# Optimization experiments

Measured on AMD Instinct MI355X. Metric: run time of the kernel, lower is better.

Reference implementation:

```python
import jax, jax.numpy as jnp
import numpy as np

N_NODES = 50000
N_EDGES = 800000
IN_DIM = 128
HID = 128
OUT_DIM = 1
N_LAYERS = 3
NUM_GRAPHS = 500
LN_EPS = 1e-5


def setup_inputs() -> dict:
    key = jax.random.key(0)
    ks = jax.random.split(key, 16)
    x = jax.random.normal(ks[0], (N_NODES, IN_DIM), dtype=jnp.float32)
    edge_index = jax.random.randint(ks[1], (2, N_EDGES), 0, N_NODES, dtype=jnp.int32)
    batch = jnp.sort(jax.random.randint(ks[2], (N_NODES,), 0, NUM_GRAPHS, dtype=jnp.int32))
    s_in = 1.0 / np.sqrt(IN_DIM)
    s_h = 1.0 / np.sqrt(HID)
    W_in = jax.random.normal(ks[3], (HID, IN_DIM), jnp.float32) * s_in
    b_in = jnp.zeros((HID,), jnp.float32)
    Wc = jax.random.normal(ks[4], (N_LAYERS, HID, HID), jnp.float32) * s_h
    bc = jnp.zeros((N_LAYERS, HID), jnp.float32)
    gamma = jnp.ones((N_LAYERS, HID), jnp.float32)
    beta = jnp.zeros((N_LAYERS, HID), jnp.float32)
    W1 = jax.random.normal(ks[5], (HID // 2, HID), jnp.float32) * s_h
    b1 = jnp.zeros((HID // 2,), jnp.float32)
    W2 = jax.random.normal(ks[6], (OUT_DIM, HID // 2), jnp.float32) * (1.0 / np.sqrt(HID // 2))
    b2 = jnp.zeros((OUT_DIM,), jnp.float32)
    return dict(x=x, edge_index=edge_index, batch=batch, W_in=W_in, b_in=b_in,
                Wc=Wc, bc=bc, gamma=gamma, beta=beta, W1=W1, b1=b1, W2=W2, b2=b2)


def _layernorm(h, g, b):
    mu = jnp.mean(h, axis=-1, keepdims=True)
    var = jnp.mean(jnp.square(h - mu), axis=-1, keepdims=True)
    return (h - mu) * jax.lax.rsqrt(var + LN_EPS) * g + b


def reference(x, edge_index, batch, W_in, b_in, Wc, bc, gamma, beta, W1, b1, W2, b2):
    n = x.shape[0]
    src, dst = edge_index[0], edge_index[1]
    # GCN symmetric normalization with self-loops: deg_i = 1 + in-degree
    deg = jax.ops.segment_sum(jnp.ones_like(src, dtype=x.dtype), dst, num_segments=n) + 1.0
    dinv = jax.lax.rsqrt(deg)                       # [N]
    enorm = (dinv[src] * dinv[dst])[:, None]        # [E,1]
    self_norm = (dinv * dinv)[:, None]              # [N,1]

    h = x @ W_in.T + b_in                           # input projection [N,H]
    for l in range(N_LAYERS):
        res = h
        hw = h @ Wc[l].T                            # GCNConv linear (no bias)
        agg = jax.ops.segment_sum(hw[src] * enorm, dst, num_segments=n)
        agg = agg + hw * self_norm + bc[l]          # self-loop term + conv bias
        h = jax.nn.relu(_layernorm(agg, gamma[l], beta[l])) + res  # dropout is identity in eval

    # global_mean_pool
    counts = jax.ops.segment_sum(jnp.ones((n,), x.dtype), batch, num_segments=NUM_GRAPHS)
    pooled = jax.ops.segment_sum(h, batch, num_segments=NUM_GRAPHS) / jnp.maximum(counts, 1.0)[:, None]

    out = jax.nn.relu(pooled @ W1.T + b1) @ W2.T + b2
    return out
```

## Files before the change

### kernel.cpp

```cpp
#include <hip/hip_runtime.h>
#include <hip/hip_bf16.h>

#define HIDDIM 128
#define CAP 4096

typedef short bf16x8 __attribute__((ext_vector_type(8)));
typedef float f32x4 __attribute__((ext_vector_type(4)));

__device__ inline unsigned short f2bf(float f) {
    unsigned u = __float_as_uint(f);
    unsigned r = (u + 0x7fffu + ((u >> 16) & 1u)) >> 16;
    return (unsigned short)r;
}
__device__ inline float bf2f(unsigned short s) {
    return __uint_as_float(((unsigned)s) << 16);
}

__global__ __launch_bounds__(256) void preproc_misc(int* __restrict__ gcursor, int nbuck,
                                                    const int* __restrict__ batch, int n, int G,
                                                    int* __restrict__ gp,
                                                    const float* __restrict__ Win,
                                                    const float* __restrict__ Wc,
                                                    unsigned short* __restrict__ Wfrag,
                                                    int nbgp) {
    int bx = blockIdx.x;
    if (bx < 2) {
        int b = bx * 256 + threadIdx.x;
        if (b < nbuck) gcursor[b] = b * CAP;
        return;
    }
    bx -= 2;
    if (bx < nbgp) {
        int i = bx * 256 + threadIdx.x;
        if (i >= n) return;
        int bi = batch[i];
        if (i == 0) {
            for (int g = 0; g <= bi; ++g) gp[g] = 0;
        } else {
            int bp = batch[i - 1];
            for (int g = bp + 1; g <= bi; ++g) gp[g] = i;
        }
        if (i == n - 1) {
            for (int g = bi + 1; g <= G; ++g) gp[g] = n;
        }
        return;
    }
    bx -= nbgp;
    int gid = bx * 256 + threadIdx.x;
    if (gid >= 4 * 16384) return;
    int m = gid >> 14;
    int r = gid & 16383;
    int t = r >> 11;
    int kk = (r >> 9) & 3;
    int lane = (r >> 3) & 63;
    int j = r & 7;
    int kg = lane >> 4, oc = lane & 15;
    int o = t * 16 + oc;
    int k = kk * 32 + kg * 8 + j;
    const float* src = (m == 0) ? Win : (Wc + (m - 1) * 16384);
    float w = src[o * 128 + k];
    unsigned short hi = f2bf(w);
    unsigned short lo = f2bf(w - bf2f(hi));
    Wfrag[m * 32768 + r] = hi;
    Wfrag[m * 32768 + 16384 + r] = lo;
}

__global__ __launch_bounds__(256) void bucket_scatter(const int* __restrict__ ei, int E,
                                                      int* __restrict__ gcursor,
                                                      unsigned* __restrict__ ebuf, int nbuck) {
    __shared__ int lcount[512];
    __shared__ int lbase[512];
    int t = threadIdx.x;
    int cb = blockIdx.x * 2048;
    lcount[t] = 0;
    lcount[t + 256] = 0;
    __syncthreads();

    int bkt[8];
    int lpos[8];
    unsigned pk[8];
#pragma unroll
    for (int j = 0; j < 8; ++j) {
        int e = cb + j * 256 + t;
        if (e < E) {
            int s_ = ei[e];
            int d_ = ei[E + e];
            bkt[j] = d_ >> 7;
            pk[j] = ((unsigned)s_ << 7) | (unsigned)(d_ & 127);
            lpos[j] = atomicAdd(&lcount[bkt[j]], 1);
        } else {
            bkt[j] = -1;
            lpos[j] = 0;
            pk[j] = 0;
        }
    }
    __syncthreads();
    for (int bb = t; bb < nbuck; bb += 256) {
        int c = lcount[bb];
        lbase[bb] = c ? atomicAdd(&gcursor[bb], c) : 0;
    }
    __syncthreads();
#pragma unroll
    for (int j = 0; j < 8; ++j) {
        if (bkt[j] >= 0) {
            unsigned idx = (unsigned)lbase[bkt[j]] + (unsigned)lpos[j];
            if (idx < (unsigned)(bkt[j] + 1) * CAP)
                ebuf[idx] = pk[j];
        }
    }
}

__global__ __launch_bounds__(256) void bucket_scan(const int* __restrict__ gcursor, int nbuck,
                                                   int* __restrict__ bptr,
                                                   int* __restrict__ rowptr, int N) {
    int t = threadIdx.x;
    int lane = t & 63, wave = t >> 6;
    int i0 = 2 * t, i1 = 2 * t + 1;
    int c0 = (i0 < nbuck) ? gcursor[i0] - i0 * CAP : 0;
    int c1 = (i1 < nbuck) ? gcursor[i1] - i1 * CAP : 0;
    int s = c0 + c1;
    int inc = s;
#pragma unroll
    for (int off = 1; off < 64; off <<= 1) {
        int u = __shfl_up(inc, off);
        if (lane >= off) inc += u;
    }
    __shared__ int wtot[4];
    if (lane == 63) wtot[wave] = inc;
    __syncthreads();
    int wbase = 0;
    for (int w = 0; w < wave; ++w) wbase += wtot[w];
    inc += wbase;
    int excl = inc - s;
    if (i0 < nbuck) bptr[i0] = excl;
    if (i1 < nbuck) bptr[i1] = excl + c0;
    if (t == 255) {
        int total = wtot[0] + wtot[1] + wtot[2] + wtot[3];
        bptr[nbuck] = total;
        rowptr[N] = total;
    }
}

__global__ __launch_bounds__(256) void csr_build(const unsigned* __restrict__ ebuf,
                                                 const int* __restrict__ bptr, int N,
                                                 int* __restrict__ rowptr,
                                                 int* __restrict__ csr_src,
                                                 float* __restrict__ dinv) {
    __shared__ int hist[128];
    __shared__ int excl[128];
    __shared__ int cur[128];
    int b = blockIdx.x;
    int t = threadIdx.x;
    int node0 = b << 7;
    int e0 = bptr[b], e1 = bptr[b + 1];
    int cnt = e1 - e0;
    if (t < 128) hist[t] = 0;
    __syncthreads();
    const unsigned* slab = ebuf + (size_t)b * CAP;
    for (int k = t; k < cnt; k += 256) atomicAdd(&hist[slab[k] & 127], 1);
    __syncthreads();
    if (t < 128) excl[t] = hist[t];
    __syncthreads();
    for (int off = 1; off < 128; off <<= 1) {
        int v = (t < 128 && t >= off) ? excl[t - off] : 0;
        __syncthreads();
        if (t < 128) excl[t] += v;
        __syncthreads();
    }
    if (t < 128) {
        int ex = excl[t] - hist[t];
        excl[t] = ex;
        cur[t] = ex;
    }
    __syncthreads();
    int nn = N - node0;
    if (nn > 128) nn = 128;
    if (t < nn) {
        rowptr[node0 + t] = e0 + excl[t];
        dinv[node0 + t] = 1.0f / sqrtf((float)hist[t] + 1.0f);
    }
    for (int k = t; k < cnt; k += 256) {
        unsigned p = slab[k];
        int dl = p & 127;
        int pos = atomicAdd(&cur[dl], 1);
        csr_src[e0 + pos] = (int)(p >> 7);
    }
}

__global__ __launch_bounds__(512) void gemm_mfma(const float* __restrict__ A,
                                                 const unsigned short* __restrict__ Wfrag,
                                                 const float* __restrict__ bias,
                                                 const float* __restrict__ scale,
                                                 void* __restrict__ Cout, int n, int use_bias,
                                                 int use_scale, int out_bf16) {
    __shared__ unsigned short sB[32768];
    int tid = threadIdx.x;
    int wave = tid >> 6;
    int lane = tid & 63;
    int wbase = blockIdx.x * 128 + wave * 16;

    {
        const float4* src = (const float4*)Wfrag;
        float4* dst = (float4*)sB;
#pragma unroll
        for (int i = 0; i < 8; ++i) dst[tid + i * 512] = src[tid + i * 512];
    }
    __syncthreads();

    f32x4 acc[8];
#pragma unroll
    for (int t = 0; t < 8; ++t) acc[t] = (f32x4){0.f, 0.f, 0.f, 0.f};

    int arow = wbase + (lane & 15);
    int kg8 = (lane >> 4) * 8;

#pragma unroll
    for (int kk = 0; kk < 4; ++kk) {
        float4 v0 = {0.f, 0.f, 0.f, 0.f}, v1 = {0.f, 0.f, 0.f, 0.f};
        if (arow < n) {
            const float* ap = A + (size_t)arow * 128 + kk * 32 + kg8;
            v0 = *(const float4*)(ap);
            v1 = *(const float4*)(ap + 4);
        }
        float fs[8] = {v0.x, v0.y, v0.z, v0.w, v1.x, v1.y, v1.z, v1.w};
        bf16x8 ahi, alo;
#pragma unroll
        for (int j = 0; j < 8; ++j) {
            unsigned short h = f2bf(fs[j]);
            ahi[j] = (short)h;
            alo[j] = (short)f2bf(fs[j] - bf2f(h));
        }
#pragma unroll
        for (int t = 0; t < 8; ++t) {
            int boff = ((t * 4 + kk) * 64 + lane) * 8;
            bf16x8 bhi = *(const bf16x8*)(sB + boff);
            bf16x8 blo = *(const bf16x8*)(sB + 16384 + boff);
            acc[t] = __builtin_amdgcn_mfma_f32_16x16x32_bf16(ahi, bhi, acc[t], 0, 0, 0);
            acc[t] = __builtin_amdgcn_mfma_f32_16x16x32_bf16(ahi, blo, acc[t], 0, 0, 0);
            acc[t] = __builtin_amdgcn_mfma_f32_16x16x32_bf16(alo, bhi, acc[t], 0, 0, 0);
        }
    }

    int colbase = lane & 15;
    int rquad = (lane >> 4) * 4;
    float bvs[8];
#pragma unroll
    for (int t = 0; t < 8; ++t) bvs[t] = use_bias ? bias[t * 16 + colbase] : 0.0f;
#pragma unroll
    for (int r = 0; r < 4; ++r) {
        int gr = wbase + rquad + r;
        if (gr >= n) continue;
        float s = use_scale ? scale[gr] : 1.0f;
        if (out_bf16) {
            unsigned short* crow = (unsigned short*)Cout + (size_t)gr * 128;
#pragma unroll
            for (int t = 0; t < 8; ++t) crow[t * 16 + colbase] = f2bf((acc[t][r] + bvs[t]) * s);
        } else {
            float* crow = (float*)Cout + (size_t)gr * 128;
#pragma unroll
            for (int t = 0; t < 8; ++t) crow[t * 16 + colbase] = (acc[t][r] + bvs[t]) * s;
        }
    }
}

__global__ __launch_bounds__(256) void gather_ln(const unsigned short* __restrict__ hws,
                                                 float* __restrict__ h,
                                                 const int* __restrict__ rowptr,
                                                 const int* __restrict__ csr_src,
                                                 const float* __restrict__ dinv,
                                                 const float* __restrict__ bc,
                                                 const float* __restrict__ gamma,
                                                 const float* __restrict__ beta, int n) {
    int wid = (blockIdx.x * 256 + threadIdx.x) >> 6;
    int lane = threadIdx.x & 63;
    if (wid >= n) return;
    int i = wid;
    float di = dinv[i];
    int e0 = rowptr[i], e1 = rowptr[i + 1];
    int c0 = lane * 2;
    const unsigned short* hb = hws + c0;

    ushort2 r0 = *(const ushort2*)(hb + (size_t)i * HIDDIM);
    float sx = bf2f(r0.x), sy = bf2f(r0.y);
    int e = e0;
    for (; e + 8 <= e1; e += 8) {
        int i0 = csr_src[e + 0], i1 = csr_src[e + 1], i2 = csr_src[e + 2], i3 = csr_src[e + 3];
        int i4 = csr_src[e + 4], i5 = csr_src[e + 5], i6 = csr_src[e + 6], i7 = csr_src[e + 7];
        ushort2 v0 = *(const ushort2*)(hb + (size_t)i0 * HIDDIM);
        ushort2 v1 = *(const ushort2*)(hb + (size_t)i1 * HIDDIM);
        ushort2 v2 = *(const ushort2*)(hb + (size_t)i2 * HIDDIM);
        ushort2 v3 = *(const ushort2*)(hb + (size_t)i3 * HIDDIM);
        ushort2 v4 = *(const ushort2*)(hb + (size_t)i4 * HIDDIM);
        ushort2 v5 = *(const ushort2*)(hb + (size_t)i5 * HIDDIM);
        ushort2 v6 = *(const ushort2*)(hb + (size_t)i6 * HIDDIM);
        ushort2 v7 = *(const ushort2*)(hb + (size_t)i7 * HIDDIM);
        sx += bf2f(v0.x); sy += bf2f(v0.y);  sx += bf2f(v1.x); sy += bf2f(v1.y);
        sx += bf2f(v2.x); sy += bf2f(v2.y);  sx += bf2f(v3.x); sy += bf2f(v3.y);
        sx += bf2f(v4.x); sy += bf2f(v4.y);  sx += bf2f(v5.x); sy += bf2f(v5.y);
        sx += bf2f(v6.x); sy += bf2f(v6.y);  sx += bf2f(v7.x); sy += bf2f(v7.y);
    }
    if (e + 4 <= e1) {
        int i0 = csr_src[e + 0], i1 = csr_src[e + 1], i2 = csr_src[e + 2], i3 = csr_src[e + 3];
        ushort2 v0 = *(const ushort2*)(hb + (size_t)i0 * HIDDIM);
        ushort2 v1 = *(const ushort2*)(hb + (size_t)i1 * HIDDIM);
        ushort2 v2 = *(const ushort2*)(hb + (size_t)i2 * HIDDIM);
        ushort2 v3 = *(const ushort2*)(hb + (size_t)i3 * HIDDIM);
        sx += bf2f(v0.x); sy += bf2f(v0.y);  sx += bf2f(v1.x); sy += bf2f(v1.y);
        sx += bf2f(v2.x); sy += bf2f(v2.y);  sx += bf2f(v3.x); sy += bf2f(v3.y);
        e += 4;
    }
    for (; e < e1; ++e) {
        int sc = csr_src[e];
        ushort2 v = *(const ushort2*)(hb + (size_t)sc * HIDDIM);
        sx += bf2f(v.x); sy += bf2f(v.y);
    }
    float2 bcv = *(const float2*)(bc + c0);
    float vx = di * sx + bcv.x;
    float vy = di * sy + bcv.y;

    float s1 = vx + vy, s2 = vx * vx + vy * vy;
#pragma unroll
    for (int off = 32; off; off >>= 1) {
        s1 += __shfl_xor(s1, off);
        s2 += __shfl_xor(s2, off);
    }
    float mu = s1 * (1.0f / 128.0f);
    float var = s2 * (1.0f / 128.0f) - mu * mu;
    float rs = 1.0f / sqrtf(var + 1e-5f);

    float2 gm = *(const float2*)(gamma + c0);
    float2 bt = *(const float2*)(beta + c0);
    float yx = fmaxf((vx - mu) * rs * gm.x + bt.x, 0.0f);
    float yy = fmaxf((vy - mu) * rs * gm.y + bt.y, 0.0f);

    float2 hv = *(float2*)(h + (size_t)i * HIDDIM + c0);
    hv.x += yx; hv.y += yy;
    *(float2*)(h + (size_t)i * HIDDIM + c0) = hv;
}

__global__ __launch_bounds__(128) void pool_mlp_kernel(const float* __restrict__ h,
                                                       const int* __restrict__ gp,
                                                       const float* __restrict__ W1,
                                                       const float* __restrict__ b1,
                                                       const float* __restrict__ W2,
                                                       const float* __restrict__ b2,
                                                       float* __restrict__ out, int G) {
    __shared__ float sp[128];
    int g = blockIdx.x;
    if (g >= G) return;
    int t = threadIdx.x;
    int s = gp[g], e = gp[g + 1];
    float a0 = 0.0f, a1 = 0.0f;
    int i = s;
    for (; i + 2 <= e; i += 2) {
        a0 += h[(size_t)i * HIDDIM + t];
        a1 += h[(size_t)(i + 1) * HIDDIM + t];
    }
    if (i < e) a0 += h[(size_t)i * HIDDIM + t];
    float cnt = fmaxf((float)(e - s), 1.0f);
    sp[t] = (a0 + a1) / cnt;
    __syncthreads();
    if (t < 64) {
        const float* wr = W1 + t * HIDDIM;
        float a = 0.0f;
#pragma unroll 8
        for (int k = 0; k < HIDDIM; k += 4) {
            float4 p = *(const float4*)(sp + k);
            float4 w = *(const float4*)(wr + k);
            a += p.x * w.x + p.y * w.y + p.z * w.z + p.w * w.w;
        }
        float h1 = fmaxf(a + b1[t], 0.0f);
        float c = h1 * W2[t];
#pragma unroll
        for (int off = 32; off; off >>= 1) c += __shfl_xor(c, off);
        if (t == 0) out[g] = c + b2[0];
    }
}

extern "C" void kernel_launch(void* const* d_in, const int* in_sizes, int n_in,
                              void* d_out, int out_size, void* d_ws, size_t ws_size,
                              hipStream_t stream) {
    const float* x      = (const float*)d_in[0];
    const int*   ei     = (const int*)d_in[1];
    const int*   batch  = (const int*)d_in[2];
    const float* W_in   = (const float*)d_in[3];
    const float* b_in   = (const float*)d_in[4];
    const float* Wc     = (const float*)d_in[5];
    const float* bc     = (const float*)d_in[6];
    const float* gamma  = (const float*)d_in[7];
    const float* beta   = (const float*)d_in[8];
    const float* W1     = (const float*)d_in[9];
    const float* b1     = (const float*)d_in[10];
    const float* W2     = (const float*)d_in[11];
    const float* b2     = (const float*)d_in[12];
    float* out = (float*)d_out;

    const int N = in_sizes[2];
    const int E = in_sizes[1] / 2;
    const int G = out_size;
    const int NBUCK = (N + 127) >> 7;

    char* ws = (char*)d_ws;
    size_t off = 0;
    auto alloc = [&](size_t bytes) {
        size_t o = off;
        off = (off + bytes + 255) & ~(size_t)255;
        return o;
    };
    int*      rowptr  = (int*)(ws + alloc((size_t)(N + 1) * 4));
    int*      csr_src = (int*)(ws + alloc((size_t)E * 4));
    float*    dinv    = (float*)(ws + alloc((size_t)N * 4));
    unsigned* ebuf    = (unsigned*)(ws + alloc((size_t)NBUCK * CAP * 4));
    int*      gcursor = (int*)(ws + alloc((size_t)NBUCK * 4));
    int*      bptr    = (int*)(ws + alloc((size_t)(NBUCK + 1) * 4));
    unsigned short* Wfrag = (unsigned short*)(ws + alloc((size_t)4 * 32768 * 2));
    float*    h       = (float*)(ws + alloc((size_t)N * 128 * 4));
    unsigned short* hws = (unsigned short*)(ws + alloc((size_t)N * 128 * 2));
    int*      gp      = (int*)(ws + alloc((size_t)(G + 1) * 4));
    (void)ws_size; (void)n_in;

    const int NBGP = (N + 255) / 256;
    const int NBPW = (4 * 16384 + 255) / 256;
    preproc_misc<<<2 + NBGP + NBPW, 256, 0, stream>>>(gcursor, NBUCK, batch, N, G, gp,
                                                      W_in, Wc, Wfrag, NBGP);
    bucket_scatter<<<(E + 2047) / 2048, 256, 0, stream>>>(ei, E, gcursor, ebuf, NBUCK);
    bucket_scan<<<1, 256, 0, stream>>>(gcursor, NBUCK, bptr, rowptr, N);
    csr_build<<<NBUCK, 256, 0, stream>>>(ebuf, bptr, N, rowptr, csr_src, dinv);

    int mblocks = (N + 127) / 128;
    gemm_mfma<<<mblocks, 512, 0, stream>>>(x, Wfrag, b_in, nullptr, h, N, 1, 0, 0);

    for (int l = 0; l < 3; ++l) {
        gemm_mfma<<<mblocks, 512, 0, stream>>>(h, Wfrag + (1 + l) * 32768, nullptr, dinv,
                                               hws, N, 0, 1, 1);
        gather_ln<<<(N + 3) / 4, 256, 0, stream>>>(hws, h, rowptr, csr_src, dinv,
                                                   bc + l * 128, gamma + l * 128,
                                                   beta + l * 128, N);
    }

    pool_mlp_kernel<<<G, 128, 0, stream>>>(h, gp, W1, b1, W2, b2, out, G);
}
```

Before: 298.1 us.

## Widen gather loads to 16B per lane and fold bucket scan into CSR build

The gather/LayerNorm kernel now splits a wave into four edge-rows of sixteen lanes, each lane loading eight bf16 values (16 bytes) per neighbor. Partial sums are reduced across rows with shuffles, which replaces many narrow 4-byte gathers with fewer wide ones. Separately, the single-block bucket_scan kernel is removed: each csr_build block recomputes its own prefix offset by summing the preceding bucket counts, saving one launch and its serialization at the cost of redundant reads. Only a quarter of the lanes now do the final LayerNorm write, and bucket counts are clamped to CAP, which slightly changes overflow handling.

Measured after the change: 298.1 us. About the same (-0.0%).

```diff
diff --git a/kernel.cpp b/kernel.cpp
--- a/kernel.cpp
+++ b/kernel.cpp
@@ -6,6 +6,7 @@
 
 typedef short bf16x8 __attribute__((ext_vector_type(8)));
 typedef float f32x4 __attribute__((ext_vector_type(4)));
+typedef unsigned short u16x8 __attribute__((ext_vector_type(8)));
 
 __device__ inline unsigned short f2bf(float f) {
     unsigned u = __float_as_uint(f);
@@ -110,52 +111,37 @@
     }
 }
 
-__global__ __launch_bounds__(256) void bucket_scan(const int* __restrict__ gcursor, int nbuck,
-                                                   int* __restrict__ bptr,
-                                                   int* __restrict__ rowptr, int N) {
-    int t = threadIdx.x;
-    int lane = t & 63, wave = t >> 6;
-    int i0 = 2 * t, i1 = 2 * t + 1;
-    int c0 = (i0 < nbuck) ? gcursor[i0] - i0 * CAP : 0;
-    int c1 = (i1 < nbuck) ? gcursor[i1] - i1 * CAP : 0;
-    int s = c0 + c1;
-    int inc = s;
-#pragma unroll
-    for (int off = 1; off < 64; off <<= 1) {
-        int u = __shfl_up(inc, off);
-        if (lane >= off) inc += u;
-    }
-    __shared__ int wtot[4];
-    if (lane == 63) wtot[wave] = inc;
-    __syncthreads();
-    int wbase = 0;
-    for (int w = 0; w < wave; ++w) wbase += wtot[w];
-    inc += wbase;
-    int excl = inc - s;
-    if (i0 < nbuck) bptr[i0] = excl;
-    if (i1 < nbuck) bptr[i1] = excl + c0;
-    if (t == 255) {
-        int total = wtot[0] + wtot[1] + wtot[2] + wtot[3];
-        bptr[nbuck] = total;
-        rowptr[N] = total;
-    }
-}
-
 __global__ __launch_bounds__(256) void csr_build(const unsigned* __restrict__ ebuf,
-                                                 const int* __restrict__ bptr, int N,
+                                                 const int* __restrict__ gcursor,
+                                                 int N, int nbuck,
                                                  int* __restrict__ rowptr,
                                                  int* __restrict__ csr_src,
                                                  float* __restrict__ dinv) {
     __shared__ int hist[128];
     __shared__ int excl[128];
     __shared__ int cur[128];
+    __shared__ int wsum[4];
+    __shared__ int sh_e0;
     int b = blockIdx.x;
     int t = threadIdx.x;
+    int partial = 0;
+    for (int j = t; j < b; j += 256) {
+        int c = gcursor[j] - j * CAP;
+        partial += (c > CAP) ? CAP : c;
+    }
+#pragma unroll
+    for (int off = 32; off; off >>= 1) partial += __shfl_xor(partial, off);
+    if ((t & 63) == 0) wsum[t >> 6] = partial;
+    if (t < 128) hist[t] = 0;
+    __syncthreads();
+    if (t == 0) sh_e0 = wsum[0] + wsum[1] + wsum[2] + wsum[3];
+    __syncthreads();
+    int e0 = sh_e0;
+    int cnt = gcursor[b] - b * CAP;
+    if (cnt > CAP) cnt = CAP;
+    if (b == nbuck - 1 && t == 0) rowptr[N] = e0 + cnt;
+
     int node0 = b << 7;
-    int e0 = bptr[b], e1 = bptr[b + 1];
-    int cnt = e1 - e0;
-    if (t < 128) hist[t] = 0;
-    __syncthreads();
     const unsigned* slab = ebuf + (size_t)b * CAP;
     for (int k = t; k < cnt; k += 256) atomicAdd(&hist[slab[k] & 127], 1);
     __syncthreads();
@@ -275,52 +261,63 @@
     int lane = threadIdx.x & 63;
     if (wid >= n) return;
     int i = wid;
+    int r = lane >> 4;
+    int c = lane & 15;
     float di = dinv[i];
     int e0 = rowptr[i], e1 = rowptr[i + 1];
-    int c0 = lane * 2;
-    const unsigned short* hb = hws + c0;
-
-    ushort2 r0 = *(const ushort2*)(hb + (size_t)i * HIDDIM);
-    float sx = bf2f(r0.x), sy = bf2f(r0.y);
+
+    float acc[8];
+#pragma unroll
+    for (int j = 0; j < 8; ++j) acc[j] = 0.0f;
+
     int e = e0;
     for (; e + 8 <= e1; e += 8) {
-        int i0 = csr_src[e + 0], i1 = csr_src[e + 1], i2 = csr_src[e + 2], i3 = csr_src[e + 3];
-        int i4 = csr_src[e + 4], i5 = csr_src[e + 5], i6 = csr_src[e + 6], i7 = csr_src[e + 7];
-        ushort2 v0 = *(const ushort2*)(hb + (size_t)i0 * HIDDIM);
-        ushort2 v1 = *(const ushort2*)(hb + (size_t)i1 * HIDDIM);
-        ushort2 v2 = *(const ushort2*)(hb + (size_t)i2 * HIDDIM);
-        ushort2 v3 = *(const ushort2*)(hb + (size_t)i3 * HIDDIM);
-        ushort2 v4 = *(const ushort2*)(hb + (size_t)i4 * HIDDIM);
-        ushort2 v5 = *(const ushort2*)(hb + (size_t)i5 * HIDDIM);
-        ushort2 v6 = *(const ushort2*)(hb + (size_t)i6 * HIDDIM);
-        ushort2 v7 = *(const ushort2*)(hb + (size_t)i7 * HIDDIM);
-        sx += bf2f(v0.x); sy += bf2f(v0.y);  sx += bf2f(v1.x); sy += bf2f(v1.y);
-        sx += bf2f(v2.x); sy += bf2f(v2.y);  sx += bf2f(v3.x); sy += bf2f(v3.y);
-        sx += bf2f(v4.x); sy += bf2f(v4.y);  sx += bf2f(v5.x); sy += bf2f(v5.y);
-        sx += bf2f(v6.x); sy += bf2f(v6.y);  sx += bf2f(v7.x); sy += bf2f(v7.y);
+        int s0 = csr_src[e + r];
+        int s1 = csr_src[e + 4 + r];
+        u16x8 v0 = *(const u16x8*)(hws + (size_t)s0 * HIDDIM + c * 8);
+        u16x8 v1 = *(const u16x8*)(hws + (size_t)s1 * HIDDIM + c * 8);
+#pragma unroll
+        for (int j = 0; j < 8; ++j) acc[j] += bf2f(v0[j]);
+#pragma unroll
+        for (int j = 0; j < 8; ++j) acc[j] += bf2f(v1[j]);
     }
     if (e + 4 <= e1) {
-        int i0 = csr_src[e + 0], i1 = csr_src[e + 1], i2 = csr_src[e + 2], i3 = csr_src[e + 3];
-        ushort2 v0 = *(const ushort2*)(hb + (size_t)i0 * HIDDIM);
-        ushort2 v1 = *(const ushort2*)(hb + (size_t)i1 * HIDDIM);
-        ushort2 v2 = *(const ushort2*)(hb + (size_t)i2 * HIDDIM);
-        ushort2 v3 = *(const ushort2*)(hb + (size_t)i3 * HIDDIM);
-        sx += bf2f(v0.x); sy += bf2f(v0.y);  sx += bf2f(v1.x); sy += bf2f(v1.y);
-        sx += bf2f(v2.x); sy += bf2f(v2.y);  sx += bf2f(v3.x); sy += bf2f(v3.y);
+        int s0 = csr_src[e + r];
+        u16x8 v0 = *(const u16x8*)(hws + (size_t)s0 * HIDDIM + c * 8);
+#pragma unroll
+        for (int j = 0; j < 8; ++j) acc[j] += bf2f(v0[j]);
         e += 4;
     }
-    for (; e < e1; ++e) {
-        int sc = csr_src[e];
-        ushort2 v = *(const ushort2*)(hb + (size_t)sc * HIDDIM);
-        sx += bf2f(v.x); sy += bf2f(v.y);
-    }
-    float2 bcv = *(const float2*)(bc + c0);
-    float vx = di * sx + bcv.x;
-    float vy = di * sy + bcv.y;
-
-    float s1 = vx + vy, s2 = vx * vx + vy * vy;
-#pragma unroll
-    for (int off = 32; off; off >>= 1) {
+    int rem = e1 - e;
+    if (r < rem) {
+        int s0 = csr_src[e + r];
+        u16x8 v0 = *(const u16x8*)(hws + (size_t)s0 * HIDDIM + c * 8);
+#pragma unroll
+        for (int j = 0; j < 8; ++j) acc[j] += bf2f(v0[j]);
+    }
+#pragma unroll
+    for (int j = 0; j < 8; ++j) {
+        acc[j] += __shfl_xor(acc[j], 16);
+        acc[j] += __shfl_xor(acc[j], 32);
+    }
+    {
+        u16x8 sv = *(const u16x8*)(hws + (size_t)i * HIDDIM + c * 8);
+#pragma unroll
+        for (int j = 0; j < 8; ++j) acc[j] += bf2f(sv[j]);
+    }
+    float4 bc0 = *(const float4*)(bc + c * 8);
+    float4 bc1 = *(const float4*)(bc + c * 8 + 4);
+    float v[8];
+    v[0] = di * acc[0] + bc0.x; v[1] = di * acc[1] + bc0.y;
+    v[2] = di * acc[2] + bc0.z; v[3] = di * acc[3] + bc0.w;
+    v[4] = di * acc[4] + bc1.x; v[5] = di * acc[5] + bc1.y;
+    v[6] = di * acc[6] + bc1.z; v[7] = di * acc[7] + bc1.w;
+
+    float s1 = 0.0f, s2 = 0.0f;
+#pragma unroll
+    for (int j = 0; j < 8; ++j) { s1 += v[j]; s2 += v[j] * v[j]; }
+#pragma unroll
+    for (int off = 1; off <= 8; off <<= 1) {
         s1 += __shfl_xor(s1, off);
         s2 += __shfl_xor(s2, off);
     }
@@ -328,14 +325,23 @@
     float var = s2 * (1.0f / 128.0f) - mu * mu;
     float rs = 1.0f / sqrtf(var + 1e-5f);
 
-    float2 gm = *(const float2*)(gamma + c0);
-    float2 bt = *(const float2*)(beta + c0);
-    float yx = fmaxf((vx - mu) * rs * gm.x + bt.x, 0.0f);
-    float yy = fmaxf((vy - mu) * rs * gm.y + bt.y, 0.0f);
-
-    float2 hv = *(float2*)(h + (size_t)i * HIDDIM + c0);
-    hv.x += yx; hv.y += yy;
-    *(float2*)(h + (size_t)i * HIDDIM + c0) = hv;
+    if (r == 0) {
+        float4 gm0 = *(const float4*)(gamma + c * 8);
+        float4 gm1 = *(const float4*)(gamma + c * 8 + 4);
+        float4 bt0 = *(const float4*)(beta + c * 8);
+        float4 bt1 = *(const float4*)(beta + c * 8 + 4);
+        float gmv[8] = {gm0.x, gm0.y, gm0.z, gm0.w, gm1.x, gm1.y, gm1.z, gm1.w};
+        float btv[8] = {bt0.x, bt0.y, bt0.z, bt0.w, bt1.x, bt1.y, bt1.z, bt1.w};
+        float* hp = h + (size_t)i * HIDDIM + c * 8;
+        float4 h0 = *(float4*)(hp);
+        float4 h1 = *(float4*)(hp + 4);
+        float hv[8] = {h0.x, h0.y, h0.z, h0.w, h1.x, h1.y, h1.z, h1.w};
+#pragma unroll
+        for (int j = 0; j < 8; ++j)
+            hv[j] += fmaxf((v[j] - mu) * rs * gmv[j] + btv[j], 0.0f);
+        *(float4*)(hp) = make_float4(hv[0], hv[1], hv[2], hv[3]);
+        *(float4*)(hp + 4) = make_float4(hv[4], hv[5], hv[6], hv[7]);
+    }
 }
 
 __global__ __launch_bounds__(128) void pool_mlp_kernel(const float* __restrict__ h,
@@ -412,7 +418,6 @@
     float*    dinv    = (float*)(ws + alloc((size_t)N * 4));
     unsigned* ebuf    = (unsigned*)(ws + alloc((size_t)NBUCK * CAP * 4));
     int*      gcursor = (int*)(ws + alloc((size_t)NBUCK * 4));
-    int*      bptr    = (int*)(ws + alloc((size_t)(NBUCK + 1) * 4));
     unsigned short* Wfrag = (unsigned short*)(ws + alloc((size_t)4 * 32768 * 2));
     float*    h       = (float*)(ws + alloc((size_t)N * 128 * 4));
     unsigned short* hws = (unsigned short*)(ws + alloc((size_t)N * 128 * 2));
@@ -424,8 +429,7 @@
     preproc_misc<<<2 + NBGP + NBPW, 256, 0, stream>>>(gcursor, NBUCK, batch, N, G, gp,
                                                       W_in, Wc, Wfrag, NBGP);
     bucket_scatter<<<(E + 2047) / 2048, 256, 0, stream>>>(ei, E, gcursor, ebuf, NBUCK);
-    bucket_scan<<<1, 256, 0, stream>>>(gcursor, NBUCK, bptr, rowptr, N);
-    csr_build<<<NBUCK, 256, 0, stream>>>(ebuf, bptr, N, rowptr, csr_src, dinv);
+    csr_build<<<NBUCK, 256, 0, stream>>>(ebuf, gcursor, N, NBUCK, rowptr, csr_src, dinv);
 
     int mblocks = (N + 127) / 128;
     gemm_mfma<<<mblocks, 512, 0, stream>>>(x, Wfrag, b_in, nullptr, h, N, 1, 0, 0);
```
